# Kernel optimization log

Hardware: AMD Instinct MI355X
Metric: run time of the kernel (lower is better)

## Reference

```python
import jax, jax.numpy as jnp
import numpy as np

PROTO_DIM = 512
PROTO_NUM = 4096
BSZ = 256
SUBTEXT_NUM = 64
TEMP = 0.9


def setup_inputs() -> dict:
    key = jax.random.key(0)
    k1, k2, k3 = jax.random.split(key, 3)
    subtexts = jax.random.normal(k1, (BSZ, SUBTEXT_NUM, PROTO_DIM), dtype=jnp.float32)
    prototype = jax.random.normal(k2, (PROTO_NUM, PROTO_DIM), dtype=jnp.float32)
    uniform = jax.random.uniform(k3, (BSZ * SUBTEXT_NUM, PROTO_NUM), dtype=jnp.float32)
    return {"subtexts": subtexts, "prototype": prototype, "uniform": uniform}


def reference(subtexts, prototype, uniform):
    # flatten: [N, D] with N = bsz * subtext_num
    flatten = subtexts.reshape(-1, PROTO_DIM)
    # dist: [N, proto_num] = flatten @ prototype.T
    dist = jnp.einsum("nd,pd->np", flatten, prototype)
    # Gumbel noise g = -log(-log(u)), matching torch F.gumbel_softmax sampling
    tiny = jnp.float32(1e-10)
    gumbel = -jnp.log(-jnp.log(uniform + tiny) + tiny)
    # noisy logits -> softmax over codebook dim (tau = curr_temp)
    soft_one_hot = jax.nn.softmax((dist + gumbel) / jnp.float32(TEMP), axis=1)
    # output: [N, D] soft codebook lookup
    output = jnp.einsum("np,pd->nd", soft_one_hot, prototype)
    proto_idx = jnp.argmax(soft_one_hot, axis=1)
    proto_loss = jnp.mean(jnp.abs(output - flatten))
    return (output, proto_loss, proto_idx)
```

## Files before the change

### kernel.cpp

```cpp
#include <hip/hip_runtime.h>
#include <math.h>

#define NROWS 16384
#define DIM   512
#define NPROTO 4096
#define TINV (1.0f / 0.9f)
#define LOSS_OFF ((size_t)NROWS * DIM)
#define IDX_OFF  ((size_t)NROWS * DIM + 1)
#define LCAP 128
#define LTHR 10.0f

typedef __attribute__((ext_vector_type(4))) int i32x4;

__global__ void zero_loss_kernel(float* out) { out[LOSS_OFF] = 0.0f; }
__global__ void zero_ws_kernel(float* wsLoss) { wsLoss[threadIdx.x] = 0.0f; }

static __device__ __forceinline__ void gl_lds16(const void* g, void* l) {
    __builtin_amdgcn_global_load_lds((const __attribute__((address_space(1))) unsigned int*)g,
                                     (__attribute__((address_space(3))) unsigned int*)l, 16, 0, 0);
}

__global__ __launch_bounds__(256)
void split_i8_kernel(const float* __restrict__ src, char* __restrict__ d1, char* __restrict__ d0,
                     float* __restrict__ dScale, int nrows)
{
    __shared__ __align__(16) char s1[32][512];
    __shared__ __align__(16) char s0[32][512];
    const int tid = threadIdx.x;
    const int row = tid >> 3;
    const int sub = tid & 7;
    const int r0 = blockIdx.x * 32;
    const float* rp = &src[(size_t)(r0 + row) * DIM + sub * 64];
    float v[64];
    float mx = 1e-20f;
#pragma unroll
    for (int i = 0; i < 16; ++i) {
        float4 f = *(const float4*)&rp[i * 4];
        v[i*4+0] = f.x; v[i*4+1] = f.y; v[i*4+2] = f.z; v[i*4+3] = f.w;
        mx = fmaxf(mx, fmaxf(fmaxf(fabsf(f.x), fabsf(f.y)), fmaxf(fabsf(f.z), fabsf(f.w))));
    }
#pragma unroll
    for (int off = 1; off < 8; off <<= 1) mx = fmaxf(mx, __shfl_xor(mx, off));
    const float s   = mx * (1.0f / 16256.0f);
    const float inv = 16256.0f / mx;
    if (sub == 0) dScale[r0 + row] = s;
#pragma unroll
    for (int i = 0; i < 64; ++i) {
        float q  = v[i] * inv;
        float a1 = rintf(q * (1.0f / 128.0f));
        float a0 = rintf(q - 128.0f * a1);
        s1[row][sub * 64 + i] = (char)(int)a1;
        s0[row][sub * 64 + i] = (char)(int)a0;
    }
    __syncthreads();
#pragma unroll
    for (int i = 0; i < 4; ++i) {
        int idx = i * 256 + tid;
        int g = idx >> 5;
        int rr = idx & 31;
        size_t o = ((size_t)g * nrows + r0 + rr) * 16;
        *(ulonglong2*)&d1[o] = *(const ulonglong2*)&s1[rr][g * 16];
        *(ulonglong2*)&d0[o] = *(const ulonglong2*)&s0[rr][g * 16];
    }
}

#define BM 32
#define BN 256
#define NCHUNK (NPROTO / BN)
#define NT 8

__global__ __launch_bounds__(256, 2)
void gemm_collect2(const float* __restrict__ U,
                   int* __restrict__ gCnt, uint2* __restrict__ gList,
                   const char* __restrict__ wsA1, const char* __restrict__ wsA0,
                   const char* __restrict__ wsP1, const char* __restrict__ wsP0,
                   const float* __restrict__ wsSA, const float* __restrict__ wsSP)
{
    __shared__ __align__(16) char sA[2][2][4][BM][16];
    __shared__ __align__(16) char sP[2][2][4][BN][16];
    __shared__ float wMax[4][BM];
    __shared__ float mRun[BM];
    __shared__ float smSA[BM];
    __shared__ int cnt[BM];

    const int tid = threadIdx.x;
    const int w = tid >> 6;
    const int lane = tid & 63;
    const int l4 = lane & 15;
    const int lh = lane >> 4;
    const int row0 = blockIdx.x * BM;

    if (tid < BM) { mRun[tid] = -1e30f; cnt[tid] = 0; smSA[tid] = wsSA[row0 + tid]; }

    const char* gp[9];
    int str9[9], fx9[9], bstr9[9];
    char* ld9[9];
#pragma unroll
    for (int si = 0; si < 9; ++si) {
        int s = w * 9 + si;
        if (s < 4) {
            int limb = s >> 1, gpair = s & 1;
            int g = gpair * 2 + (lane >> 5);
            gp[si]  = (limb ? wsA0 : wsA1) + ((size_t)g * NROWS + row0 + (lane & 31)) * 16;
            str9[si] = 4 * NROWS * 16;
            fx9[si]  = -NT * 4 * NROWS * 16;
            ld9[si]  = &sA[0][limb][gpair * 2][0][0] + (size_t)lane * 16;
            bstr9[si] = 2 * 4 * BM * 16;
        } else {
            int p = s - 4;
            int limb = p >> 4, rem = p & 15, g = rem >> 2, q = rem & 3;
            gp[si]  = (limb ? wsP0 : wsP1) + ((size_t)g * NPROTO + q * 64 + lane) * 16;
            str9[si] = 4 * NPROTO * 16;
            fx9[si]  = -NT * 4 * NPROTO * 16 + BN * 16;
            ld9[si]  = &sP[0][limb][g][q * 64][0] + (size_t)lane * 16;
            bstr9[si] = 2 * 4 * BN * 16;
        }
    }
#define DO_STAGE(b) { _Pragma("unroll") for (int si = 0; si < 9; ++si) { \
        gl_lds16(gp[si], ld9[si] + ((b) ? bstr9[si] : 0)); gp[si] += str9[si]; } }
#define DO_FIXUP() { _Pragma("unroll") for (int si = 0; si < 9; ++si) gp[si] += fx9[si]; }

    i32x4 c11[2][4], c10[2][4], c01[2][4];
    auto COMPUTE = [&](int cur) {
        i32x4 a1[2], a0[2], b1[4], b0[4];
#pragma unroll
        for (int mf = 0; mf < 2; ++mf) {
            a1[mf] = *(const i32x4*)&sA[cur][0][lh][mf * 16 + l4][0];
            a0[mf] = *(const i32x4*)&sA[cur][1][lh][mf * 16 + l4][0];
        }
#pragma unroll
        for (int nf = 0; nf < 4; ++nf) {
            b1[nf] = *(const i32x4*)&sP[cur][0][lh][w * 64 + nf * 16 + l4][0];
            b0[nf] = *(const i32x4*)&sP[cur][1][lh][w * 64 + nf * 16 + l4][0];
        }
#pragma unroll
        for (int mf = 0; mf < 2; ++mf)
#pragma unroll
            for (int nf = 0; nf < 4; ++nf) {
                c11[mf][nf] = __builtin_amdgcn_mfma_i32_16x16x64_i8(a1[mf], b1[nf], c11[mf][nf], 0, 0, 0);
                c10[mf][nf] = __builtin_amdgcn_mfma_i32_16x16x64_i8(a1[mf], b0[nf], c10[mf][nf], 0, 0, 0);
                c01[mf][nf] = __builtin_amdgcn_mfma_i32_16x16x64_i8(a0[mf], b1[nf], c01[mf][nf], 0, 0, 0);
            }
    };

    DO_STAGE(0);
    __syncthreads();

    for (int ch = 0; ch < NCHUNK; ++ch) {
        const int pbase = ch * BN;
        float spv[4];
#pragma unroll
        for (int nf = 0; nf < 4; ++nf) spv[nf] = wsSP[pbase + w * 64 + nf * 16 + l4];
#pragma unroll
        for (int mf = 0; mf < 2; ++mf)
#pragma unroll
            for (int nf = 0; nf < 4; ++nf) {
                c11[mf][nf] = i32x4{0,0,0,0}; c10[mf][nf] = i32x4{0,0,0,0}; c01[mf][nf] = i32x4{0,0,0,0};
            }

#pragma unroll 2
        for (int t = 0; t < NT; ++t) {
            const int cur = t & 1;
            if (t < NT - 1) {
                DO_STAGE(cur ^ 1);
            } else if (ch + 1 < NCHUNK) {
                DO_FIXUP(); DO_STAGE(cur ^ 1);
            }
            COMPUTE(cur);
            __syncthreads();
        }

        float zf[2][4][4];
#pragma unroll
        for (int mf = 0; mf < 2; ++mf) {
            const int rb = row0 + mf * 16 + lh * 4;
#pragma unroll
            for (int nf = 0; nf < 4; ++nf)
#pragma unroll
                for (int r = 0; r < 4; ++r) {
                    float dist = smSA[mf * 16 + lh * 4 + r] * spv[nf] *
                                 (16384.0f * (float)c11[mf][nf][r] +
                                  128.0f * ((float)c10[mf][nf][r] + (float)c01[mf][nf][r]));
                    float u = U[(size_t)(rb + r) * NPROTO + pbase + w * 64 + nf * 16 + l4];
                    float g = -__logf(-__logf(u + 1e-10f) + 1e-10f);
                    zf[mf][nf][r] = (dist + g) * TINV;
                }
        }
#pragma unroll
        for (int mf = 0; mf < 2; ++mf) {
            float rm[4];
#pragma unroll
            for (int r = 0; r < 4; ++r)
                rm[r] = fmaxf(fmaxf(zf[mf][0][r], zf[mf][1][r]), fmaxf(zf[mf][2][r], zf[mf][3][r]));
#pragma unroll
            for (int off = 1; off < 16; off <<= 1)
#pragma unroll
                for (int r = 0; r < 4; ++r) rm[r] = fmaxf(rm[r], __shfl_xor(rm[r], off));
#pragma unroll
            for (int r = 0; r < 4; ++r) {
                const int rl = mf * 16 + lh * 4 + r;
                float thrv = fmaxf(mRun[rl], rm[r]) - LTHR;
#pragma unroll
                for (int nf = 0; nf < 4; ++nf) {
                    float z = zf[mf][nf][r];
                    if (z > thrv) {
                        int pos = atomicAdd(&cnt[rl], 1);
                        if (pos < LCAP) {
                            uint2 en; en.x = __float_as_uint(z);
                            en.y = (unsigned)(pbase + w * 64 + nf * 16 + l4);
                            gList[(size_t)(row0 + rl) * LCAP + pos] = en;
                        }
                    }
                }
            }
            if (l4 == 0)
#pragma unroll
                for (int r = 0; r < 4; ++r) wMax[w][mf * 16 + lh * 4 + r] = rm[r];
        }
        __syncthreads();
        if (tid < BM) {
            float gm = fmaxf(fmaxf(wMax[0][tid], wMax[1][tid]), fmaxf(wMax[2][tid], wMax[3][tid]));
            mRun[tid] = fmaxf(mRun[tid], gm);
        }
        __syncthreads();
    }
#undef DO_STAGE
#undef DO_FIXUP

    __syncthreads();
    if (tid < BM) gCnt[row0 + tid] = cnt[tid];
}

__global__ __launch_bounds__(256)
void finish_kernel(const float* __restrict__ A, const float* __restrict__ Pr,
                   const float* __restrict__ U, float* __restrict__ out,
                   const int* __restrict__ gCnt, const uint2* __restrict__ gList,
                   float* __restrict__ wsLoss)
{
    __shared__ uint2 sl[4][LCAP];
    const int tid = threadIdx.x;
    const int lane = tid & 63;
    const int wv = tid >> 6;
    const int row = blockIdx.x * 4 + wv;
    const int c = min(gCnt[row], LCAP);
    const uint2* lst = &gList[(size_t)row * LCAP];

    for (int e = lane; e < c; e += 64) sl[wv][e] = lst[e];

    float M = -1e30f;
    for (int e = lane; e < c; e += 64) M = fmaxf(M, __uint_as_float(sl[wv][e].x));
#pragma unroll
    for (int off = 1; off < 64; off <<= 1) M = fmaxf(M, __shfl_xor(M, off));
    const float cutoff = M - LTHR;

    float L = 0.f, bz = -1e30f; int bi = 1 << 30;
    for (int e = lane; e < c; e += 64) {
        float z = __uint_as_float(sl[wv][e].x); int p = (int)sl[wv][e].y;
        if (z > cutoff) {
            L += __expf(z - M);
            if (z > bz || (z == bz && p < bi)) { bz = z; bi = p; }
        }
    }
#pragma unroll
    for (int off = 1; off < 64; off <<= 1) {
        L += __shfl_xor(L, off);
        float oz = __shfl_xor(bz, off); int oi = __shfl_xor(bi, off);
        if (oz > bz || (oz == bz && oi < bi)) { bz = oz; bi = oi; }
    }

    float bestz = -1e30f; int bestp = 1 << 30;
    const float* ap = &A[(size_t)row * DIM];
    for (int e = lane; e < c; e += 64) {
        float z = __uint_as_float(sl[wv][e].x);
        if (z > bz - 3.0f) {
            int p = (int)sl[wv][e].y;
            const float* pp = &Pr[(size_t)p * DIM];
            float d = 0.f;
            for (int k = 0; k < DIM; k += 4) {
                float4 av = *(const float4*)&ap[k];
                float4 pv = *(const float4*)&pp[k];
                d = fmaf(av.x, pv.x, d);
                d = fmaf(av.y, pv.y, d);
                d = fmaf(av.z, pv.z, d);
                d = fmaf(av.w, pv.w, d);
            }
            float u = U[(size_t)row * NPROTO + p];
            float g = -logf(-logf(u + 1e-10f) + 1e-10f);
            float zz = (d + g) * (1.0f / 0.9f);
            if (zz > bestz || (zz == bestz && p < bestp)) { bestz = zz; bestp = p; }
        }
    }
#pragma unroll
    for (int off = 1; off < 64; off <<= 1) {
        float oz = __shfl_xor(bestz, off); int oi = __shfl_xor(bestp, off);
        if (oz > bestz || (oz == bestz && oi < bestp)) { bestz = oz; bestp = oi; }
    }
    if (lane == 0) out[IDX_OFF + row] = (float)bestp;

    const float Li = 1.0f / L;
    float oA[8], oB[8];
#pragma unroll
    for (int q = 0; q < 8; ++q) { oA[q] = 0.f; oB[q] = 0.f; }
    for (int e = 0; e < c; e += 2) {
        const uint2 ea = sl[wv][e];
        const uint2 eb = sl[wv][(e + 1 < c) ? e + 1 : e];
        const float za = __uint_as_float(ea.x);
        const float zb = __uint_as_float(eb.x);
        const float wa = (za > cutoff) ? __expf(za - M) * Li : 0.f;
        const float wb = (e + 1 < c && zb > cutoff) ? __expf(zb - M) * Li : 0.f;
        const float* pa = &Pr[(size_t)ea.y * DIM + lane * 8];
        const float* pb = &Pr[(size_t)eb.y * DIM + lane * 8];
        float4 a0 = *(const float4*)pa;
        float4 a1 = *(const float4*)(pa + 4);
        float4 b0 = *(const float4*)pb;
        float4 b1 = *(const float4*)(pb + 4);
        oA[0] = fmaf(wa, a0.x, oA[0]); oA[1] = fmaf(wa, a0.y, oA[1]);
        oA[2] = fmaf(wa, a0.z, oA[2]); oA[3] = fmaf(wa, a0.w, oA[3]);
        oA[4] = fmaf(wa, a1.x, oA[4]); oA[5] = fmaf(wa, a1.y, oA[5]);
        oA[6] = fmaf(wa, a1.z, oA[6]); oA[7] = fmaf(wa, a1.w, oA[7]);
        oB[0] = fmaf(wb, b0.x, oB[0]); oB[1] = fmaf(wb, b0.y, oB[1]);
        oB[2] = fmaf(wb, b0.z, oB[2]); oB[3] = fmaf(wb, b0.w, oB[3]);
        oB[4] = fmaf(wb, b1.x, oB[4]); oB[5] = fmaf(wb, b1.y, oB[5]);
        oB[6] = fmaf(wb, b1.z, oB[6]); oB[7] = fmaf(wb, b1.w, oB[7]);
    }
    float o[8];
#pragma unroll
    for (int q = 0; q < 8; ++q) o[q] = oA[q] + oB[q];

    const float* fr = &A[(size_t)row * DIM + lane * 8];
    float4 f0 = *(const float4*)fr; float4 f1 = *(const float4*)(fr + 4);
    *(float4*)&out[(size_t)row * DIM + lane * 8]     = make_float4(o[0], o[1], o[2], o[3]);
    *(float4*)&out[(size_t)row * DIM + lane * 8 + 4] = make_float4(o[4], o[5], o[6], o[7]);
    float lossAcc = fabsf(o[0]-f0.x) + fabsf(o[1]-f0.y) + fabsf(o[2]-f0.z) + fabsf(o[3]-f0.w)
                  + fabsf(o[4]-f1.x) + fabsf(o[5]-f1.y) + fabsf(o[6]-f1.z) + fabsf(o[7]-f1.w);
#pragma unroll
    for (int off = 1; off < 64; off <<= 1) lossAcc += __shfl_xor(lossAcc, off);
    if (lane == 0) atomicAdd(&wsLoss[blockIdx.x & 63], lossAcc * (1.0f / ((float)NROWS * (float)DIM)));
}

__global__ void loss_final_kernel(const float* __restrict__ wsLoss, float* __restrict__ out)
{
    float s = wsLoss[threadIdx.x];
#pragma unroll
    for (int off = 1; off < 64; off <<= 1) s += __shfl_xor(s, off);
    if (threadIdx.x == 0) out[LOSS_OFF] = s;
}

#define FCAP 192
#define FTHR 20.0f

__global__ __launch_bounds__(256, 1)
void attr_proto_fused_valu(const float* __restrict__ A, const float* __restrict__ Pr,
                           const float* __restrict__ U, float* __restrict__ out)
{
    __shared__ __align__(16) float As[64][64 + 4];
    __shared__ __align__(16) float Bs[128][64 + 4];
    __shared__ float hZ[64][FCAP];
    __shared__ unsigned short hI[64][FCAP];
    __shared__ int cnt[64];
    __shared__ float mArr[64];
    __shared__ float lArr[64];
    __shared__ int pruneFlag;

    const int tid = threadIdx.x;
    const int tx = tid & 31;
    const int ty = tid >> 5;
    const int row0 = blockIdx.x * 64;

    for (int r = tid; r < 64; r += 256) cnt[r] = 0;
    if (tid == 0) pruneFlag = 0;

    float m[8], l[8], bz[8];
    int bi[8];
#pragma unroll
    for (int i = 0; i < 8; ++i) { m[i] = -INFINITY; l[i] = 0.0f; bz[i] = -INFINITY; bi[i] = 0; }
    __syncthreads();

    for (int ch = 0; ch < 32; ++ch) {
        const int pbase = ch * 128;
        float acc[8][4];
#pragma unroll
        for (int i = 0; i < 8; ++i)
#pragma unroll
            for (int j = 0; j < 4; ++j) acc[i][j] = 0.0f;

        for (int kk = 0; kk < DIM; kk += 64) {
#pragma unroll
            for (int q = 0; q < 4; ++q) {
                int lin = tid + q * 256;
                int lr = lin >> 4; int kq = (lin & 15) << 2;
                *(float4*)&As[lr][kq] = *(const float4*)&A[(size_t)(row0 + lr) * DIM + kk + kq];
            }
#pragma unroll
            for (int q = 0; q < 8; ++q) {
                int lin = tid + q * 256;
                int pr = lin >> 4; int kq = (lin & 15) << 2;
                *(float4*)&Bs[pr][kq] = *(const float4*)&Pr[(size_t)(pbase + pr) * DIM + kk + kq];
            }
            __syncthreads();
#pragma unroll 4
            for (int k4 = 0; k4 < 64; k4 += 4) {
                float4 av[8], bv[4];
#pragma unroll
                for (int i = 0; i < 8; ++i) av[i] = *(const float4*)&As[ty * 8 + i][k4];
#pragma unroll
                for (int j = 0; j < 4; ++j) bv[j] = *(const float4*)&Bs[tx + 32 * j][k4];
#pragma unroll
                for (int i = 0; i < 8; ++i)
#pragma unroll
                    for (int j = 0; j < 4; ++j) {
                        acc[i][j] += av[i].x * bv[j].x; acc[i][j] += av[i].y * bv[j].y;
                        acc[i][j] += av[i].z * bv[j].z; acc[i][j] += av[i].w * bv[j].w;
                    }
            }
            __syncthreads();
        }
#pragma unroll
        for (int i = 0; i < 8; ++i) {
            const int ri = ty * 8 + i;
            const size_t urow = (size_t)(row0 + ri) * NPROTO + pbase;
            float z[4]; float lmax = -INFINITY;
#pragma unroll
            for (int j = 0; j < 4; ++j) {
                float u = U[urow + tx + 32 * j];
                float g = -logf(-logf(u + 1e-10f) + 1e-10f);
                z[j] = (acc[i][j] + g) * TINV;
                lmax = fmaxf(lmax, z[j]);
            }
#pragma unroll
            for (int off = 16; off; off >>= 1) lmax = fmaxf(lmax, __shfl_xor(lmax, off, 32));
            const float mn = fmaxf(m[i], lmax);
            float s = 0.0f;
#pragma unroll
            for (int j = 0; j < 4; ++j) s += expf(z[j] - mn);
#pragma unroll
            for (int off = 16; off; off >>= 1) s += __shfl_xor(s, off, 32);
            l[i] = l[i] * expf(m[i] - mn) + s;
            m[i] = mn;
#pragma unroll
            for (int j = 0; j < 4; ++j) {
                const int p = pbase + tx + 32 * j;
                if (z[j] > bz[i]) { bz[i] = z[j]; bi[i] = p; }
                if (z[j] > mn - FTHR) {
                    int pos = atomicAdd(&cnt[ri], 1);
                    if (pos < FCAP) { hZ[ri][pos] = z[j]; hI[ri][pos] = (unsigned short)p; }
                }
            }
            if (tx == 0) {
                mArr[ri] = mn;
                if (cnt[ri] > 64) atomicOr(&pruneFlag, 1);
            }
        }
        __syncthreads();
        if (pruneFlag) {
            for (int r = 0; r < 64; ++r) {
                const int c0 = min(cnt[r], FCAP);
                if (c0 > 64) {
                    const float thr = mArr[r] - FTHR;
                    float ez = 0.0f; int ei = 0; bool keep = false;
                    if (tid < c0) { ez = hZ[r][tid]; ei = hI[r][tid]; keep = (ez > thr); }
                    __syncthreads();
                    if (tid == 0) cnt[r] = 0;
                    __syncthreads();
                    if (keep) { int pos = atomicAdd(&cnt[r], 1); hZ[r][pos] = ez; hI[r][pos] = (unsigned short)ei; }
                    __syncthreads();
                }
            }
            if (tid == 0) pruneFlag = 0;
            __syncthreads();
        }
    }
#pragma unroll
    for (int i = 0; i < 8; ++i) {
        const int ri = ty * 8 + i;
        float vz = bz[i]; int vi = bi[i];
#pragma unroll
        for (int off = 16; off; off >>= 1) {
            float oz = __shfl_xor(vz, off, 32); int oi = __shfl_xor(vi, off, 32);
            if (oz > vz || (oz == vz && oi < vi)) { vz = oz; vi = oi; }
        }
        if (tx == 0) { lArr[ri] = l[i]; out[IDX_OFF + row0 + ri] = (float)vi; }
    }
    __syncthreads();

    const int wv = tid >> 6;
    const int lane = tid & 63;
    float lossAcc = 0.0f;
    for (int r = wv; r < 64; r += 4) {
        const int grow = row0 + r;
        const int c = min(cnt[r], FCAP);
        const float mm = mArr[r];
        const float li = 1.0f / lArr[r];
        float o[8];
#pragma unroll
        for (int q = 0; q < 8; ++q) o[q] = 0.0f;
        for (int e = 0; e < c; ++e) {
            const float wg = expf(hZ[r][e] - mm) * li;
            const float* pp = &Pr[(size_t)hI[r][e] * DIM + lane * 8];
            float4 p0 = *(const float4*)pp; float4 p1 = *(const float4*)(pp + 4);
            o[0] += wg * p0.x; o[1] += wg * p0.y; o[2] += wg * p0.z; o[3] += wg * p0.w;
            o[4] += wg * p1.x; o[5] += wg * p1.y; o[6] += wg * p1.z; o[7] += wg * p1.w;
        }
        const float* fr = &A[(size_t)grow * DIM + lane * 8];
        float4 f0 = *(const float4*)fr; float4 f1 = *(const float4*)(fr + 4);
        *(float4*)&out[(size_t)grow * DIM + lane * 8]     = make_float4(o[0], o[1], o[2], o[3]);
        *(float4*)&out[(size_t)grow * DIM + lane * 8 + 4] = make_float4(o[4], o[5], o[6], o[7]);
        lossAcc += fabsf(o[0]-f0.x) + fabsf(o[1]-f0.y) + fabsf(o[2]-f0.z) + fabsf(o[3]-f0.w)
                 + fabsf(o[4]-f1.x) + fabsf(o[5]-f1.y) + fabsf(o[6]-f1.z) + fabsf(o[7]-f1.w);
    }
#pragma unroll
    for (int off = 32; off; off >>= 1) lossAcc += __shfl_xor(lossAcc, off, 64);
    if (lane == 0) atomicAdd(&out[LOSS_OFF], lossAcc * (1.0f / ((float)NROWS * (float)DIM)));
}

extern "C" void kernel_launch(void* const* d_in, const int* in_sizes, int n_in,
                              void* d_out, int out_size, void* d_ws, size_t ws_size,
                              hipStream_t stream)
{
    const float* A  = (const float*)d_in[0];
    const float* Pr = (const float*)d_in[1];
    const float* U  = (const float*)d_in[2];
    float* out = (float*)d_out;

    const size_t szA = (size_t)NROWS * DIM;
    const size_t szP = (size_t)NPROTO * DIM;
    const size_t scBytes  = (size_t)(NROWS + NPROTO) * sizeof(float);
    const size_t listBytes = (size_t)NROWS * LCAP * sizeof(uint2);
    const size_t cntBytes = (size_t)NROWS * sizeof(int);
    const size_t need = 2 * szA + 2 * szP + scBytes + listBytes + cntBytes + 64 * sizeof(float);

    if (ws_size >= need) {
        char*  wsA1 = (char*)d_ws;
        char*  wsA0 = wsA1 + szA;
        char*  wsP1 = wsA0 + szA;
        char*  wsP0 = wsP1 + szP;
        float* wsSA = (float*)(wsP0 + szP);
        float* wsSP = wsSA + NROWS;
        uint2* gList = (uint2*)(wsSP + NPROTO);
        int*   gCnt  = (int*)((char*)gList + listBytes);
        float* wsLoss = (float*)((char*)gCnt + cntBytes);
        split_i8_kernel<<<NROWS / 32, 256, 0, stream>>>(A, wsA1, wsA0, wsSA, NROWS);
        split_i8_kernel<<<NPROTO / 32, 256, 0, stream>>>(Pr, wsP1, wsP0, wsSP, NPROTO);
        zero_ws_kernel<<<1, 64, 0, stream>>>(wsLoss);
        gemm_collect2<<<NROWS / BM, 256, 0, stream>>>(U, gCnt, gList,
                                                      wsA1, wsA0, wsP1, wsP0, wsSA, wsSP);
        finish_kernel<<<NROWS / 4, 256, 0, stream>>>(A, Pr, U, out, gCnt, gList, wsLoss);
        loss_final_kernel<<<1, 64, 0, stream>>>(wsLoss, out);
    } else {
        zero_loss_kernel<<<1, 1, 0, stream>>>(out);
        attr_proto_fused_valu<<<NROWS / 64, 256, 0, stream>>>(A, Pr, U, out);
    }
}
```

Baseline: 408.3 us.

## Shrink int8 GEMM tile to 16x128 and raise occupancy to four blocks per CU

Cuts the row tile from 32 to 16 and the prototype chunk from 256 to 128. It also remaps the async global-to-LDS load slots (5 or 4 per wave instead of 9) and reduces the per-wave MFMA accumulators to one M fragment and two N fragments. The launch bound rises to 4 blocks per CU and the grid doubles, so more waves are available to hide latency. The cost is less data reuse per tile: each prototype chunk is reloaded by twice as many blocks, more barriers run per unit of work, and the per-chunk epilogue runs twice as often.

New measurement: 443.4 us. +8.6%, slower.

```diff
diff --git a/kernel.cpp b/kernel.cpp
--- a/kernel.cpp
+++ b/kernel.cpp
@@ -64,13 +64,13 @@
     }
 }
 
-#define BM 32
-#define BN 256
+#define BM 16
+#define BN 128
 #define NCHUNK (NPROTO / BN)
 #define NT 8
 
-__global__ __launch_bounds__(256, 2)
-void gemm_collect2(const float* __restrict__ U,
+__global__ __launch_bounds__(256, 4)
+void gemm_collect3(const float* __restrict__ U,
                    int* __restrict__ gCnt, uint2* __restrict__ gList,
                    const char* __restrict__ wsA1, const char* __restrict__ wsA0,
                    const char* __restrict__ wsP1, const char* __restrict__ wsP0,
@@ -92,55 +92,51 @@
 
     if (tid < BM) { mRun[tid] = -1e30f; cnt[tid] = 0; smSA[tid] = wsSA[row0 + tid]; }
 
-    const char* gp[9];
-    int str9[9], fx9[9], bstr9[9];
-    char* ld9[9];
-#pragma unroll
-    for (int si = 0; si < 9; ++si) {
-        int s = w * 9 + si;
-        if (s < 4) {
-            int limb = s >> 1, gpair = s & 1;
-            int g = gpair * 2 + (lane >> 5);
-            gp[si]  = (limb ? wsA0 : wsA1) + ((size_t)g * NROWS + row0 + (lane & 31)) * 16;
-            str9[si] = 4 * NROWS * 16;
-            fx9[si]  = -NT * 4 * NROWS * 16;
-            ld9[si]  = &sA[0][limb][gpair * 2][0][0] + (size_t)lane * 16;
-            bstr9[si] = 2 * 4 * BM * 16;
+    const int nslot = (w < 2) ? 5 : 4;
+    const char* gp[5];
+    int str5[5], fx5[5], bstr5[5];
+    char* ld5[5];
+#pragma unroll
+    for (int si = 0; si < 5; ++si) {
+        int s = si * 4 + w;
+        if (s >= 18) continue;
+        if (s < 2) {
+            int limb = s;
+            gp[si]  = (limb ? wsA0 : wsA1) + ((size_t)(lane >> 4) * NROWS + row0 + (lane & 15)) * 16;
+            str5[si] = 4 * NROWS * 16;
+            fx5[si]  = -NT * 4 * NROWS * 16;
+            ld5[si]  = &sA[0][limb][0][0][0] + (size_t)lane * 16;
+            bstr5[si] = 2 * 4 * BM * 16;
         } else {
-            int p = s - 4;
-            int limb = p >> 4, rem = p & 15, g = rem >> 2, q = rem & 3;
-            gp[si]  = (limb ? wsP0 : wsP1) + ((size_t)g * NPROTO + q * 64 + lane) * 16;
-            str9[si] = 4 * NPROTO * 16;
-            fx9[si]  = -NT * 4 * NPROTO * 16 + BN * 16;
-            ld9[si]  = &sP[0][limb][g][q * 64][0] + (size_t)lane * 16;
-            bstr9[si] = 2 * 4 * BN * 16;
-        }
-    }
-#define DO_STAGE(b) { _Pragma("unroll") for (int si = 0; si < 9; ++si) { \
-        gl_lds16(gp[si], ld9[si] + ((b) ? bstr9[si] : 0)); gp[si] += str9[si]; } }
-#define DO_FIXUP() { _Pragma("unroll") for (int si = 0; si < 9; ++si) gp[si] += fx9[si]; }
-
-    i32x4 c11[2][4], c10[2][4], c01[2][4];
+            int p = s - 2;
+            int limb = p >> 3, rem = p & 7, g = rem >> 1, half = rem & 1;
+            gp[si]  = (limb ? wsP0 : wsP1) + ((size_t)g * NPROTO + half * 64 + lane) * 16;
+            str5[si] = 4 * NPROTO * 16;
+            fx5[si]  = -NT * 4 * NPROTO * 16 + BN * 16;
+            ld5[si]  = &sP[0][limb][g][half * 64][0] + (size_t)lane * 16;
+            bstr5[si] = 2 * 4 * BN * 16;
+        }
+    }
+#define DO_STAGE(b) { _Pragma("unroll") for (int si = 0; si < 5; ++si) { if (si < nslot) { \
+        gl_lds16(gp[si], ld5[si] + ((b) ? bstr5[si] : 0)); gp[si] += str5[si]; } } }
+#define DO_FIXUP() { _Pragma("unroll") for (int si = 0; si < 5; ++si) { if (si < nslot) gp[si] += fx5[si]; } }
+
+    i32x4 c11[2], c10[2], c01[2];
     auto COMPUTE = [&](int cur) {
-        i32x4 a1[2], a0[2], b1[4], b0[4];
-#pragma unroll
-        for (int mf = 0; mf < 2; ++mf) {
-            a1[mf] = *(const i32x4*)&sA[cur][0][lh][mf * 16 + l4][0];
-            a0[mf] = *(const i32x4*)&sA[cur][1][lh][mf * 16 + l4][0];
-        }
-#pragma unroll
-        for (int nf = 0; nf < 4; ++nf) {
-            b1[nf] = *(const i32x4*)&sP[cur][0][lh][w * 64 + nf * 16 + l4][0];
-            b0[nf] = *(const i32x4*)&sP[cur][1][lh][w * 64 + nf * 16 + l4][0];
-        }
-#pragma unroll
-        for (int mf = 0; mf < 2; ++mf)
-#pragma unroll
-            for (int nf = 0; nf < 4; ++nf) {
-                c11[mf][nf] = __builtin_amdgcn_mfma_i32_16x16x64_i8(a1[mf], b1[nf], c11[mf][nf], 0, 0, 0);
-                c10[mf][nf] = __builtin_amdgcn_mfma_i32_16x16x64_i8(a1[mf], b0[nf], c10[mf][nf], 0, 0, 0);
-                c01[mf][nf] = __builtin_amdgcn_mfma_i32_16x16x64_i8(a0[mf], b1[nf], c01[mf][nf], 0, 0, 0);
-            }
+        i32x4 a1, a0, b1[2], b0[2];
+        a1 = *(const i32x4*)&sA[cur][0][lh][l4][0];
+        a0 = *(const i32x4*)&sA[cur][1][lh][l4][0];
+#pragma unroll
+        for (int nf = 0; nf < 2; ++nf) {
+            b1[nf] = *(const i32x4*)&sP[cur][0][lh][w * 32 + nf * 16 + l4][0];
+            b0[nf] = *(const i32x4*)&sP[cur][1][lh][w * 32 + nf * 16 + l4][0];
+        }
+#pragma unroll
+        for (int nf = 0; nf < 2; ++nf) {
+            c11[nf] = __builtin_amdgcn_mfma_i32_16x16x64_i8(a1, b1[nf], c11[nf], 0, 0, 0);
+            c10[nf] = __builtin_amdgcn_mfma_i32_16x16x64_i8(a1, b0[nf], c10[nf], 0, 0, 0);
+            c01[nf] = __builtin_amdgcn_mfma_i32_16x16x64_i8(a0, b1[nf], c01[nf], 0, 0, 0);
+        }
     };
 
     DO_STAGE(0);
@@ -148,15 +144,13 @@
 
     for (int ch = 0; ch < NCHUNK; ++ch) {
         const int pbase = ch * BN;
-        float spv[4];
-#pragma unroll
-        for (int nf = 0; nf < 4; ++nf) spv[nf] = wsSP[pbase + w * 64 + nf * 16 + l4];
-#pragma unroll
-        for (int mf = 0; mf < 2; ++mf)
-#pragma unroll
-            for (int nf = 0; nf < 4; ++nf) {
-                c11[mf][nf] = i32x4{0,0,0,0}; c10[mf][nf] = i32x4{0,0,0,0}; c01[mf][nf] = i32x4{0,0,0,0};
-            }
+        float spv[2];
+#pragma unroll
+        for (int nf = 0; nf < 2; ++nf) spv[nf] = wsSP[pbase + w * 32 + nf * 16 + l4];
+#pragma unroll
+        for (int nf = 0; nf < 2; ++nf) {
+            c11[nf] = i32x4{0,0,0,0}; c10[nf] = i32x4{0,0,0,0}; c01[nf] = i32x4{0,0,0,0};
+        }
 
 #pragma unroll 2
         for (int t = 0; t < NT; ++t) {
@@ -170,44 +164,39 @@
             __syncthreads();
         }
 
-        float zf[2][4][4];
-#pragma unroll
-        for (int mf = 0; mf < 2; ++mf) {
-            const int rb = row0 + mf * 16 + lh * 4;
-#pragma unroll
-            for (int nf = 0; nf < 4; ++nf)
-#pragma unroll
-                for (int r = 0; r < 4; ++r) {
-                    float dist = smSA[mf * 16 + lh * 4 + r] * spv[nf] *
-                                 (16384.0f * (float)c11[mf][nf][r] +
-                                  128.0f * ((float)c10[mf][nf][r] + (float)c01[mf][nf][r]));
-                    float u = U[(size_t)(rb + r) * NPROTO + pbase + w * 64 + nf * 16 + l4];
-                    float g = -__logf(-__logf(u + 1e-10f) + 1e-10f);
-                    zf[mf][nf][r] = (dist + g) * TINV;
-                }
-        }
-#pragma unroll
-        for (int mf = 0; mf < 2; ++mf) {
+        float zf[2][4];
+#pragma unroll
+        for (int nf = 0; nf < 2; ++nf)
+#pragma unroll
+            for (int r = 0; r < 4; ++r) {
+                const int rl = lh * 4 + r;
+                float dist = smSA[rl] * spv[nf] *
+                             (16384.0f * (float)c11[nf][r] +
+                              128.0f * ((float)c10[nf][r] + (float)c01[nf][r]));
+                float u = U[(size_t)(row0 + rl) * NPROTO + pbase + w * 32 + nf * 16 + l4];
+                float g = -__logf(-__logf(u + 1e-10f) + 1e-10f);
+                zf[nf][r] = (dist + g) * TINV;
+            }
+        {
             float rm[4];
 #pragma unroll
-            for (int r = 0; r < 4; ++r)
-                rm[r] = fmaxf(fmaxf(zf[mf][0][r], zf[mf][1][r]), fmaxf(zf[mf][2][r], zf[mf][3][r]));
+            for (int r = 0; r < 4; ++r) rm[r] = fmaxf(zf[0][r], zf[1][r]);
 #pragma unroll
             for (int off = 1; off < 16; off <<= 1)
 #pragma unroll
                 for (int r = 0; r < 4; ++r) rm[r] = fmaxf(rm[r], __shfl_xor(rm[r], off));
 #pragma unroll
             for (int r = 0; r < 4; ++r) {
-                const int rl = mf * 16 + lh * 4 + r;
+                const int rl = lh * 4 + r;
                 float thrv = fmaxf(mRun[rl], rm[r]) - LTHR;
 #pragma unroll
-                for (int nf = 0; nf < 4; ++nf) {
-                    float z = zf[mf][nf][r];
+                for (int nf = 0; nf < 2; ++nf) {
+                    float z = zf[nf][r];
                     if (z > thrv) {
                         int pos = atomicAdd(&cnt[rl], 1);
                         if (pos < LCAP) {
                             uint2 en; en.x = __float_as_uint(z);
-                            en.y = (unsigned)(pbase + w * 64 + nf * 16 + l4);
+                            en.y = (unsigned)(pbase + w * 32 + nf * 16 + l4);
                             gList[(size_t)(row0 + rl) * LCAP + pos] = en;
                         }
                     }
@@ -215,7 +204,7 @@
             }
             if (l4 == 0)
 #pragma unroll
-                for (int r = 0; r < 4; ++r) wMax[w][mf * 16 + lh * 4 + r] = rm[r];
+                for (int r = 0; r < 4; ++r) wMax[w][lh * 4 + r] = rm[r];
         }
         __syncthreads();
         if (tid < BM) {
@@ -542,7 +531,7 @@
         split_i8_kernel<<<NROWS / 32, 256, 0, stream>>>(A, wsA1, wsA0, wsSA, NROWS);
         split_i8_kernel<<<NPROTO / 32, 256, 0, stream>>>(Pr, wsP1, wsP0, wsSP, NPROTO);
         zero_ws_kernel<<<1, 64, 0, stream>>>(wsLoss);
-        gemm_collect2<<<NROWS / BM, 256, 0, stream>>>(U, gCnt, gList,
+        gemm_collect3<<<NROWS / BM, 256, 0, stream>>>(U, gCnt, gList,
                                                       wsA1, wsA0, wsP1, wsP0, wsSA, wsSP);
         finish_kernel<<<NROWS / 4, 256, 0, stream>>>(A, Pr, U, out, gCnt, gList, wsLoss);
         loss_final_kernel<<<1, 64, 0, stream>>>(wsLoss, out);
```
